# Kernel optimization log

Hardware: AMD Instinct MI355X
Metric: run time of the kernel (lower is better)

The kernel has to match this reference:

```python
import jax, jax.numpy as jnp
import numpy as np

H = 1024          # hidden_size
NH = 16           # num_attention_heads
HD = H // NH      # head_size
EPS = 1e-5


def setup_inputs() -> dict:
    key = jax.random.key(0)
    ks = jax.random.split(key, 5)
    # xavier_uniform bound for Linear(in, out): sqrt(6/(in+out))
    b_qkv = float(np.sqrt(6.0 / (H + 3 * H)))
    b_out = float(np.sqrt(6.0 / (H + H)))
    return {
        "hidden_states": jax.random.normal(ks[0], (2, 2048, H), dtype=jnp.float32),
        "ln_gamma": jnp.ones((H,), jnp.float32),
        "ln_beta": jnp.zeros((H,), jnp.float32),
        "W_qkv": jax.random.uniform(ks[1], (3 * H, H), jnp.float32, -b_qkv, b_qkv),
        "b_qkv": jnp.zeros((3 * H,), jnp.float32),
        "W_out": jax.random.uniform(ks[2], (H, H), jnp.float32, -b_out, b_out),
        "b_out": jnp.zeros((H,), jnp.float32),
    }


def _attn_block(x, ln_gamma, ln_beta, W_qkv, b_qkv, W_out, b_out):
    B, S, _ = x.shape
    # Pre-LN
    mu = jnp.mean(x, axis=-1, keepdims=True)
    var = jnp.mean(jnp.square(x - mu), axis=-1, keepdims=True)
    xn = (x - mu) / jnp.sqrt(var + EPS) * ln_gamma + ln_beta
    # fused QKV projection: [B,S,3H]
    qkv = jnp.einsum("bsh,oh->bso", xn, W_qkv) + b_qkv
    qkv = qkv.reshape(B, S, 3, NH, HD).transpose(2, 0, 3, 1, 4)  # [3,B,NH,S,HD]
    q, k, v = qkv[0], qkv[1], qkv[2]
    scores = jnp.einsum("bhqd,bhkd->bhqk", q, k) / jnp.sqrt(jnp.asarray(HD, x.dtype))
    probs = jax.nn.softmax(scores, axis=-1)
    ctx = jnp.einsum("bhqk,bhkd->bhqd", probs, v)
    ctx = ctx.transpose(0, 2, 1, 3).reshape(B, S, H)
    out = jnp.einsum("bsh,oh->bso", ctx, W_out) + b_out  # dropout: eval mode = identity
    return x + out


def reference(hidden_states, ln_gamma, ln_beta, W_qkv, b_qkv, W_out, b_out):
    return _attn_block(hidden_states, ln_gamma, ln_beta, W_qkv, b_qkv, W_out, b_out)
```

## Files before the change

### kernel.cpp

```cpp
#include <hip/hip_runtime.h>
#include <stdint.h>

typedef unsigned short u16;
typedef __attribute__((ext_vector_type(8))) short bf16x8;
typedef __attribute__((ext_vector_type(4))) float f32x4;
typedef __attribute__((ext_vector_type(16))) float f32x16;
typedef __attribute__((ext_vector_type(4))) unsigned int u32x4;
typedef __attribute__((ext_vector_type(2))) unsigned int u32x2;
typedef __attribute__((ext_vector_type(4))) unsigned short u16x4;

#define QSCALE 0.18033688011112042f

typedef __attribute__((address_space(1))) const void gvoid;
typedef __attribute__((address_space(3))) void svoid;

__device__ __forceinline__ void cp16(const u16* g, u16* l) {
    __builtin_amdgcn_global_load_lds((gvoid*)g, (svoid*)l, 16, 0, 0);
}

__device__ __forceinline__ u16 f2bf(float f) {
    uint32_t u = __float_as_uint(f);
    u += 0x7fff + ((u >> 16) & 1);
    return (u16)(u >> 16);
}

__device__ __forceinline__ uint32_t pack_bf2(float lo, float hi) {
    uint32_t a = __float_as_uint(lo) + 0x8000u;
    uint32_t b = __float_as_uint(hi) + 0x8000u;
    return __builtin_amdgcn_perm(b, a, 0x07060302);
}

__device__ __forceinline__ f32x16 zero16() {
    f32x16 v;
    #pragma unroll
    for (int i = 0; i < 16; i++) v[i] = 0.f;
    return v;
}

__global__ __launch_bounds__(256) void k_pre(const float* __restrict__ X,
                                             const float* __restrict__ gam,
                                             const float* __restrict__ bet,
                                             u16* __restrict__ XN,
                                             const float* __restrict__ Wqkv, u16* __restrict__ Wq,
                                             const float* __restrict__ Wout, u16* __restrict__ Wo) {
    __shared__ float red[8];
    const int bid = blockIdx.x;
    if (bid < 4096) {
        int t = bid;
        const float4* xp = (const float4*)(X + (size_t)t * 1024);
        float4 x = xp[threadIdx.x];
        float s  = x.x + x.y + x.z + x.w;
        float s2 = x.x*x.x + x.y*x.y + x.z*x.z + x.w*x.w;
        #pragma unroll
        for (int off = 1; off < 64; off <<= 1) {
            s  += __shfl_xor(s,  off, 64);
            s2 += __shfl_xor(s2, off, 64);
        }
        int lane = threadIdx.x & 63, w = threadIdx.x >> 6;
        if (lane == 0) { red[w] = s; red[w + 4] = s2; }
        __syncthreads();
        s  = red[0] + red[1] + red[2] + red[3];
        s2 = red[4] + red[5] + red[6] + red[7];
        float mu  = s * (1.0f / 1024.0f);
        float var = s2 * (1.0f / 1024.0f) - mu * mu;
        float rin = rsqrtf(var + 1e-5f);
        float4 g = ((const float4*)gam)[threadIdx.x];
        float4 b = ((const float4*)bet)[threadIdx.x];
        u16x4 o;
        o.x = f2bf((x.x - mu) * rin * g.x + b.x);
        o.y = f2bf((x.y - mu) * rin * g.y + b.y);
        o.z = f2bf((x.z - mu) * rin * g.z + b.z);
        o.w = f2bf((x.w - mu) * rin * g.w + b.w);
        *(u16x4*)(XN + (size_t)t * 1024 + threadIdx.x * 4) = o;
    } else {
        int i = (bid - 4096) * 256 + threadIdx.x;
        const float* src; u16* dst;
        if (i < 786432) { src = Wqkv; dst = Wq; }
        else            { i -= 786432; src = Wout; dst = Wo; }
        float4 v = ((const float4*)src)[i];
        u16x4 o;
        o.x = f2bf(v.x); o.y = f2bf(v.y); o.z = f2bf(v.z); o.w = f2bf(v.w);
        ((u16x4*)dst)[i] = o;
    }
}

__device__ __forceinline__ void gemm_bt_tile(const u16* __restrict__ A, const u16* __restrict__ Bm,
                                             int m0, int n0, u16* As, u16* Bs, f32x4 acc[4][4]) {
    const int tid = threadIdx.x;
    const int lane = tid & 63;
    const int wv = tid >> 6;
    const int qi = lane & 15, g = lane >> 4, swz = qi & 7;
    const int wr = (wv >> 1) * 64, wc = (wv & 1) * 64;
    #pragma unroll
    for (int mi = 0; mi < 4; mi++)
        #pragma unroll
        for (int ni = 0; ni < 4; ni++) acc[mi][ni] = (f32x4){0.f, 0.f, 0.f, 0.f};

    const int row_in = tid >> 3;
    const int cs = (tid & 7) ^ (row_in & 7);
    for (int k0 = 0; k0 < 1024; k0 += 64) {
        __syncthreads();
        #pragma unroll
        for (int i = 0; i < 4; i++) {
            int row = i * 32 + row_in;
            cp16(A  + (size_t)(m0 + row) * 1024 + k0 + cs * 8, As + (i * 256 + wv * 64) * 8);
            cp16(Bm + (size_t)(n0 + row) * 1024 + k0 + cs * 8, Bs + (i * 256 + wv * 64) * 8);
        }
        __syncthreads();
        #pragma unroll
        for (int ks = 0; ks < 2; ks++) {
            bf16x8 af[4], bf[4];
            #pragma unroll
            for (int mi = 0; mi < 4; mi++)
                af[mi] = *(const bf16x8*)(As + (wr + mi * 16 + qi) * 64 + ((ks * 4 + g) ^ swz) * 8);
            #pragma unroll
            for (int ni = 0; ni < 4; ni++)
                bf[ni] = *(const bf16x8*)(Bs + (wc + ni * 16 + qi) * 64 + ((ks * 4 + g) ^ swz) * 8);
            #pragma unroll
            for (int mi = 0; mi < 4; mi++)
                #pragma unroll
                for (int ni = 0; ni < 4; ni++)
                    acc[mi][ni] = __builtin_amdgcn_mfma_f32_16x16x32_bf16(af[mi], bf[ni], acc[mi][ni], 0, 0, 0);
        }
    }
}


#define CFENCE asm volatile("" ::: "memory")
#define BARX() do { CFENCE; __builtin_amdgcn_s_barrier(); CFENCE; } while (0)
#define LGKM0() asm volatile("s_waitcnt lgkmcnt(0)" ::: "memory")

__global__ __launch_bounds__(512, 2) void k_qkv(const u16* __restrict__ XN, const u16* __restrict__ Wq,
                                                const float* __restrict__ bqkv,
                                                u16* __restrict__ Q, u16* __restrict__ K,
                                                u16* __restrict__ Vt) {
    __shared__ __align__(16) u16 SMEM[65536];
    const int tid = threadIdx.x;
    const int lane = tid & 63, w = tid >> 6;
    const int qi = lane & 15, g = lane >> 4, swz = qi & 7;
    const int wr = (w >> 2) * 128, wc = (w & 3) * 64;

    const int id = blockIdx.x;
    const int sw = (id & 7) * 24 + (id >> 3);
    const int n0 = (sw % 12) * 256;
    const int m0 = (sw / 12) * 256;

    const int laneRow = lane >> 3, laneCg = lane & 7;
    const int cs = laneCg ^ laneRow;
    const int aw = (w & 3) * 8 + (w >> 2) * 128;
    const u16* gA = XN + (size_t)(m0 + aw + laneRow) * 1024 + cs * 8;
    const u16* gB = Wq + (size_t)(n0 + w * 8 + laneRow) * 1024 + cs * 8;

#define SM_A(s) (SMEM + (s) * 32768)
#define SM_B(s) (SMEM + (s) * 32768 + 16384)
#define STAGE_A(tau, q, s) cp16(gA + (size_t)(q) * 32 * 1024 + (tau) * 64, SM_A(s) + ((q) * 32 + aw) * 64)
#define STAGE_B(tau, part, s)                                                                       \
    do { cp16(gB + (size_t)(part) * 128 * 1024 + (tau) * 64, SM_B(s) + ((part) * 128 + w * 8) * 64); \
         cp16(gB + (size_t)((part) * 128 + 64) * 1024 + (tau) * 64,                                  \
              SM_B(s) + ((part) * 128 + 64 + w * 8) * 64); } while (0)

    f32x4 acc[8][4];
    #pragma unroll
    for (int mi = 0; mi < 8; mi++)
        #pragma unroll
        for (int ni = 0; ni < 4; ni++) acc[mi][ni] = (f32x4){0.f, 0.f, 0.f, 0.f};
    bf16x8 bf[4][2];

    STAGE_B(0, 0, 0); STAGE_B(0, 1, 0);
    STAGE_A(0, 0, 0); STAGE_A(0, 1, 0); STAGE_A(0, 2, 0); STAGE_A(0, 3, 0);
    STAGE_B(1, 0, 1); STAGE_B(1, 1, 1);
    STAGE_A(1, 0, 1); STAGE_A(1, 1, 1);
    asm volatile("s_waitcnt vmcnt(6)" ::: "memory");
    BARX();

#define PHASE_A(q)                                                                                   \
    bf16x8 af[2][2];                                                                                 \
    _Pragma("unroll") for (int m2 = 0; m2 < 2; m2++)                                                 \
    _Pragma("unroll") for (int ks = 0; ks < 2; ks++)                                                 \
        af[m2][ks] = *(const bf16x8*)(as_ + (wr + ((q) * 2 + m2) * 16 + qi) * 64 + (((ks * 4 + g) ^ swz)) * 8);

#define DO_MFMA(q)                                                                                   \
    __builtin_amdgcn_s_setprio(1);                                                                   \
    _Pragma("unroll") for (int m2 = 0; m2 < 2; m2++)                                                 \
    _Pragma("unroll") for (int ni = 0; ni < 4; ni++) {                                               \
        acc[(q) * 2 + m2][ni] = __builtin_amdgcn_mfma_f32_16x16x32_bf16(af[m2][0], bf[ni][0], acc[(q) * 2 + m2][ni], 0, 0, 0); \
        acc[(q) * 2 + m2][ni] = __builtin_amdgcn_mfma_f32_16x16x32_bf16(af[m2][1], bf[ni][1], acc[(q) * 2 + m2][ni], 0, 0, 0); \
    }                                                                                                \
    __builtin_amdgcn_s_setprio(0);

    for (int t = 0; t < 16; t++) {
        const int s = t & 1;
        const u16* as_ = SM_A(s);
        const u16* bs_ = SM_B(s);
        {
            PHASE_A(0)
            #pragma unroll
            for (int ni = 0; ni < 4; ni++)
                #pragma unroll
                for (int ks = 0; ks < 2; ks++)
                    bf[ni][ks] = *(const bf16x8*)(bs_ + (wc + ni * 16 + qi) * 64 + ((ks * 4 + g) ^ swz) * 8);
            if (t < 15) { STAGE_A(t + 1, 2, s ^ 1); STAGE_A(t + 1, 3, s ^ 1); }
            BARX(); LGKM0();
            DO_MFMA(0)
            BARX();
        }
        {
            PHASE_A(1)
            if (t < 14) STAGE_B(t + 2, 0, s);
            BARX(); LGKM0();
            DO_MFMA(1)
            BARX();
        }
        {
            PHASE_A(2)
            if (t < 14) STAGE_B(t + 2, 1, s);
            BARX(); LGKM0();
            DO_MFMA(2)
            BARX();
        }
        {
            PHASE_A(3)
            if (t < 14) { STAGE_A(t + 2, 0, s); STAGE_A(t + 2, 1, s); }
            BARX(); LGKM0();
            DO_MFMA(3)
            if (t < 14) { asm volatile("s_waitcnt vmcnt(6)" ::: "memory"); }
            else        { asm volatile("s_waitcnt vmcnt(0)" ::: "memory"); }
            BARX();
        }
    }

    if (n0 < 2048) {
        const int which = n0 >> 10;
        u16* base = which ? K : Q;
        const float scale = which ? 1.0f : QSCALE;
        #pragma unroll
        for (int mi = 0; mi < 8; mi++)
            #pragma unroll
            for (int ni = 0; ni < 4; ni++)
                #pragma unroll
                for (int i = 0; i < 4; i++) {
                    int m = m0 + wr + mi * 16 + (g * 4 + i);
                    int n = n0 + wc + ni * 16 + qi;
                    float v = (acc[mi][ni][i] + bqkv[n]) * scale;
                    int b = m >> 11, ss = m & 2047;
                    int hh = (n >> 6) & 15, d = n & 63;
                    base[((size_t)(b * 16 + hh) * 2048 + ss) * 64 + d] = f2bf(v);
                }
    } else {
        u16* Tw = SMEM + w * 4352;
        const int head = (n0 + wc - 2048) >> 6;
        const int b = m0 >> 11;
        #pragma unroll
        for (int h = 0; h < 2; h++) {
            #pragma unroll
            for (int mi2 = 0; mi2 < 4; mi2++)
                #pragma unroll
                for (int ni = 0; ni < 4; ni++) {
                    int mi = h * 4 + mi2;
                    int n = n0 + wc + ni * 16 + qi;
                    float bq = bqkv[n];
                    u16x4 pk;
                    pk.x = f2bf(acc[mi][ni][0] + bq);
                    pk.y = f2bf(acc[mi][ni][1] + bq);
                    pk.z = f2bf(acc[mi][ni][2] + bq);
                    pk.w = f2bf(acc[mi][ni][3] + bq);
                    *(u16x4*)(Tw + (ni * 16 + qi) * 68 + mi2 * 16 + g * 4) = pk;
                }
            int s0 = (m0 + wr + h * 64) & 2047;
            u16* vrow = Vt + (size_t)(b * 16 + head) * 64 * 2048 + s0 + qi * 4;
            #pragma unroll
            for (int dd = 0; dd < 16; dd++) {
                int d = dd * 4 + g;
                u16x4 val = *(const u16x4*)(Tw + d * 68 + qi * 4);
                *(u16x4*)(vrow + (size_t)d * 2048) = val;
            }
        }
    }
#undef SM_A
#undef SM_B
#undef STAGE_A
#undef STAGE_B
#undef PHASE_A
#undef DO_MFMA
}

__global__ __launch_bounds__(256) void k_attn(const u16* __restrict__ Q, const u16* __restrict__ K,
                                              const u16* __restrict__ Vt, u16* __restrict__ CTX) {
    __shared__ __align__(16) u16 Ks[2][64 * 64];
    __shared__ __align__(16) u16 Vs[2][64 * 64];
    const int id = blockIdx.x;
    const int bh = (id & 7) * 4 + ((id >> 3) & 3);
    const int q0 = (id >> 5) * 128;
    const int lane = threadIdx.x & 63, w = threadIdx.x >> 6;
    const int l = lane & 31, h = lane >> 5;
    const u16* Qp = Q  + (size_t)bh * (2048 * 64);
    const u16* Kp = K  + (size_t)bh * (2048 * 64);
    const u16* Vp = Vt + (size_t)bh * (64 * 2048);

    const int r0 = w * 8 + (lane >> 3);
    const int cs = (lane & 7) ^ (r0 & 7);
    const u16* kgp = Kp + (size_t)r0 * 64 + cs * 8;
    const u16* vgp = Vp + (size_t)r0 * 2048 + cs * 8;

    bf16x8 bq[4];
    {
        const u16* qb = Qp + (size_t)(q0 + w * 32 + l) * 64 + h * 8;
        #pragma unroll
        for (int dk = 0; dk < 4; dk++) bq[dk] = *(const bf16x8*)(qb + dk * 16);
    }
    float lsA = 0.f, lsB = 0.f;
    f32x16 od0 = zero16(), od1 = zero16();

    cp16(kgp,              Ks[0] + w * 512);
    cp16(kgp + 32 * 64,    Ks[0] + w * 512 + 2048);
    cp16(vgp,              Vs[0] + w * 512);
    cp16(vgp + 32 * 2048,  Vs[0] + w * 512 + 2048);

    for (int t = 0; t < 32; ++t) {
        __syncthreads();
        if (t < 31) {
            const int nb = (t + 1) & 1;
            cp16(kgp + 4096,             Ks[nb] + w * 512);
            cp16(kgp + 4096 + 32 * 64,   Ks[nb] + w * 512 + 2048);
            cp16(vgp + 64,               Vs[nb] + w * 512);
            cp16(vgp + 64 + 32 * 2048,   Vs[nb] + w * 512 + 2048);
        }
        kgp += 4096; vgp += 64;
        const u16* ksp = Ks[t & 1];
        const u16* vsp = Vs[t & 1];

        f32x16 sv0 = zero16(), sv1 = zero16();
        __builtin_amdgcn_s_setprio(1);
        #pragma unroll
        for (int dk = 0; dk < 4; dk++) {
            bf16x8 ak0 = *(const bf16x8*)(ksp + (l) * 64      + ((2 * dk + h) ^ (l & 7)) * 8);
            bf16x8 ak1 = *(const bf16x8*)(ksp + (32 + l) * 64 + ((2 * dk + h) ^ (l & 7)) * 8);
            sv0 = __builtin_amdgcn_mfma_f32_32x32x16_bf16(ak0, bq[dk], sv0, 0, 0, 0);
            sv1 = __builtin_amdgcn_mfma_f32_32x32x16_bf16(ak1, bq[dk], sv1, 0, 0, 0);
        }
        __builtin_amdgcn_s_setprio(0);

        uint32_t y[2][2][4];
#define SM_PACK(SV, KG, LS)                                                   \
        _Pragma("unroll")                                                     \
        for (int s = 0; s < 4; s++)                                           \
            _Pragma("unroll")                                                 \
            for (int p = 0; p < 2; p++) {                                     \
                float e0 = __builtin_amdgcn_exp2f(SV[4 * s + 2 * p]);         \
                float e1 = __builtin_amdgcn_exp2f(SV[4 * s + 2 * p + 1]);     \
                LS += e0 + e1;                                                \
                y[KG][p][s] = pack_bf2(e0, e1);                               \
            }
        SM_PACK(sv0, 0, lsA)
        SM_PACK(sv1, 1, lsB)
#undef SM_PACK

        #pragma unroll
        for (int m = 0; m < 4; m++) {
            const int kg = m >> 1, mt = m & 1;
            u32x2 r0s = __builtin_amdgcn_permlane32_swap(y[kg][0][2 * mt], y[kg][0][2 * mt + 1], false, false);
            u32x2 r1s = __builtin_amdgcn_permlane32_swap(y[kg][1][2 * mt], y[kg][1][2 * mt + 1], false, false);
            u32x4 bw = {r0s.x, r1s.x, r0s.y, r1s.y};
            bf16x8 bp = *(const bf16x8*)&bw;
            bf16x8 av0 = *(const bf16x8*)(vsp + (l) * 64      + ((2 * m + h) ^ (l & 7)) * 8);
            bf16x8 av1 = *(const bf16x8*)(vsp + (32 + l) * 64 + ((2 * m + h) ^ (l & 7)) * 8);
            __builtin_amdgcn_s_setprio(1);
            od0 = __builtin_amdgcn_mfma_f32_32x32x16_bf16(av0, bp, od0, 0, 0, 0);
            od1 = __builtin_amdgcn_mfma_f32_32x32x16_bf16(av1, bp, od1, 0, 0, 0);
            __builtin_amdgcn_s_setprio(0);
        }
    }

    float lsum = lsA + lsB;
    lsum += __shfl_xor(lsum, 32, 64);
    float inv = 1.0f / lsum;
    const int b = bh >> 4, hh = bh & 15;
    size_t m = (size_t)b * 2048 + q0 + w * 32 + l;
    u16* cp = CTX + m * 1024 + hh * 64;
    #pragma unroll
    for (int s = 0; s < 4; s++) {
        u16x4 o;
        o.x = f2bf(od0[4 * s + 0] * inv); o.y = f2bf(od0[4 * s + 1] * inv);
        o.z = f2bf(od0[4 * s + 2] * inv); o.w = f2bf(od0[4 * s + 3] * inv);
        *(u16x4*)(cp + 8 * s + 4 * h) = o;
        o.x = f2bf(od1[4 * s + 0] * inv); o.y = f2bf(od1[4 * s + 1] * inv);
        o.z = f2bf(od1[4 * s + 2] * inv); o.w = f2bf(od1[4 * s + 3] * inv);
        *(u16x4*)(cp + 32 + 8 * s + 4 * h) = o;
    }
}

__global__ __launch_bounds__(256) void k_out(const u16* __restrict__ CTX, const u16* __restrict__ Wo,
                                             const float* __restrict__ bout, const float* __restrict__ X,
                                             float* __restrict__ OUT) {
    __shared__ __align__(16) u16 As[128 * 64], Bs[128 * 64];
    f32x4 acc[4][4];
    const int m0 = blockIdx.y * 128, n0 = blockIdx.x * 128;
    gemm_bt_tile(CTX, Wo, m0, n0, As, Bs, acc);
    const int lane = threadIdx.x & 63, wid = threadIdx.x >> 6;
    const int wr = (wid >> 1) * 64, wc = (wid & 1) * 64;
    #pragma unroll
    for (int mi = 0; mi < 4; mi++)
        #pragma unroll
        for (int ni = 0; ni < 4; ni++)
            #pragma unroll
            for (int i = 0; i < 4; i++) {
                size_t m = m0 + wr + mi * 16 + ((lane >> 4) * 4 + i);
                int n = n0 + wc + ni * 16 + (lane & 15);
                OUT[m * 1024 + n] = acc[mi][ni][i] + bout[n] + X[m * 1024 + n];
            }
}

extern "C" void kernel_launch(void* const* d_in, const int* in_sizes, int n_in,
                              void* d_out, int out_size, void* d_ws, size_t ws_size,
                              hipStream_t stream) {
    const float* X    = (const float*)d_in[0];
    const float* gam  = (const float*)d_in[1];
    const float* bet  = (const float*)d_in[2];
    const float* Wqkv = (const float*)d_in[3];
    const float* bqkv = (const float*)d_in[4];
    const float* Wout = (const float*)d_in[5];
    const float* bout = (const float*)d_in[6];
    float* OUT = (float*)d_out;

    u16* XN  = (u16*)d_ws;
    u16* Q   = XN  + (size_t)4 * 1024 * 1024;
    u16* K   = Q   + (size_t)4 * 1024 * 1024;
    u16* Vt  = K   + (size_t)4 * 1024 * 1024;
    u16* CTX = Vt  + (size_t)4 * 1024 * 1024;
    u16* Wq  = CTX + (size_t)4 * 1024 * 1024;
    u16* Wo  = Wq  + (size_t)3 * 1024 * 1024;

    k_pre<<<8192, 256, 0, stream>>>(X, gam, bet, XN, Wqkv, Wq, Wout, Wo);
    k_qkv<<<192, 512, 0, stream>>>(XN, Wq, bqkv, Q, K, Vt);
    k_attn<<<512, 256, 0, stream>>>(Q, K, Vt, CTX);
    k_out<<<dim3(8, 32), 256, 0, stream>>>(CTX, Wo, bout, X, OUT);
}
```

Before: 194.6 us.

## Split attention key tile across wave pairs and double the grid

Each attention block now handles 64 queries instead of 128. The two waves sharing a 32-query group each process half of every 64-key tile. Their partial outputs and row sums are reduced through shared memory at the end, and the grid is doubled to 1024 blocks with a launch bound of 4 blocks per SIMD. This raises parallelism and occupancy on the 256-CU part, but each block now reloads the full K/V stream for only half as many queries, which doubles global K/V traffic and adds a reduction step.

```diff
diff --git a/kernel.cpp b/kernel.cpp
--- a/kernel.cpp
+++ b/kernel.cpp
@@ -284,15 +284,16 @@
 #undef DO_MFMA
 }
 
-__global__ __launch_bounds__(256) void k_attn(const u16* __restrict__ Q, const u16* __restrict__ K,
-                                              const u16* __restrict__ Vt, u16* __restrict__ CTX) {
+__global__ __launch_bounds__(256, 4) void k_attn(const u16* __restrict__ Q, const u16* __restrict__ K,
+                                                 const u16* __restrict__ Vt, u16* __restrict__ CTX) {
     __shared__ __align__(16) u16 Ks[2][64 * 64];
     __shared__ __align__(16) u16 Vs[2][64 * 64];
     const int id = blockIdx.x;
     const int bh = (id & 7) * 4 + ((id >> 3) & 3);
-    const int q0 = (id >> 5) * 128;
+    const int q0 = (id >> 5) * 64;
     const int lane = threadIdx.x & 63, w = threadIdx.x >> 6;
     const int l = lane & 31, h = lane >> 5;
+    const int qg = w >> 1, kh = w & 1;
     const u16* Qp = Q  + (size_t)bh * (2048 * 64);
     const u16* Kp = K  + (size_t)bh * (2048 * 64);
     const u16* Vp = Vt + (size_t)bh * (64 * 2048);
@@ -304,11 +305,11 @@
 
     bf16x8 bq[4];
     {
-        const u16* qb = Qp + (size_t)(q0 + w * 32 + l) * 64 + h * 8;
+        const u16* qb = Qp + (size_t)(q0 + qg * 32 + l) * 64 + h * 8;
         #pragma unroll
         for (int dk = 0; dk < 4; dk++) bq[dk] = *(const bf16x8*)(qb + dk * 16);
     }
-    float lsA = 0.f, lsB = 0.f;
+    float ls = 0.f;
     f32x16 od0 = zero16(), od1 = zero16();
 
     cp16(kgp,              Ks[0] + w * 512);
@@ -329,41 +330,34 @@
         const u16* ksp = Ks[t & 1];
         const u16* vsp = Vs[t & 1];
 
-        f32x16 sv0 = zero16(), sv1 = zero16();
+        f32x16 sv = zero16();
         __builtin_amdgcn_s_setprio(1);
         #pragma unroll
         for (int dk = 0; dk < 4; dk++) {
-            bf16x8 ak0 = *(const bf16x8*)(ksp + (l) * 64      + ((2 * dk + h) ^ (l & 7)) * 8);
-            bf16x8 ak1 = *(const bf16x8*)(ksp + (32 + l) * 64 + ((2 * dk + h) ^ (l & 7)) * 8);
-            sv0 = __builtin_amdgcn_mfma_f32_32x32x16_bf16(ak0, bq[dk], sv0, 0, 0, 0);
-            sv1 = __builtin_amdgcn_mfma_f32_32x32x16_bf16(ak1, bq[dk], sv1, 0, 0, 0);
+            bf16x8 ak = *(const bf16x8*)(ksp + (kh * 32 + l) * 64 + ((2 * dk + h) ^ (l & 7)) * 8);
+            sv = __builtin_amdgcn_mfma_f32_32x32x16_bf16(ak, bq[dk], sv, 0, 0, 0);
         }
         __builtin_amdgcn_s_setprio(0);
 
-        uint32_t y[2][2][4];
-#define SM_PACK(SV, KG, LS)                                                   \
-        _Pragma("unroll")                                                     \
-        for (int s = 0; s < 4; s++)                                           \
-            _Pragma("unroll")                                                 \
-            for (int p = 0; p < 2; p++) {                                     \
-                float e0 = __builtin_amdgcn_exp2f(SV[4 * s + 2 * p]);         \
-                float e1 = __builtin_amdgcn_exp2f(SV[4 * s + 2 * p + 1]);     \
-                LS += e0 + e1;                                                \
-                y[KG][p][s] = pack_bf2(e0, e1);                               \
+        uint32_t y[2][4];
+        #pragma unroll
+        for (int s = 0; s < 4; s++)
+            #pragma unroll
+            for (int p = 0; p < 2; p++) {
+                float e0 = __builtin_amdgcn_exp2f(sv[4 * s + 2 * p]);
+                float e1 = __builtin_amdgcn_exp2f(sv[4 * s + 2 * p + 1]);
+                ls += e0 + e1;
+                y[p][s] = pack_bf2(e0, e1);
             }
-        SM_PACK(sv0, 0, lsA)
-        SM_PACK(sv1, 1, lsB)
-#undef SM_PACK
-
-        #pragma unroll
-        for (int m = 0; m < 4; m++) {
-            const int kg = m >> 1, mt = m & 1;
-            u32x2 r0s = __builtin_amdgcn_permlane32_swap(y[kg][0][2 * mt], y[kg][0][2 * mt + 1], false, false);
-            u32x2 r1s = __builtin_amdgcn_permlane32_swap(y[kg][1][2 * mt], y[kg][1][2 * mt + 1], false, false);
+
+        #pragma unroll
+        for (int mt = 0; mt < 2; mt++) {
+            u32x2 r0s = __builtin_amdgcn_permlane32_swap(y[0][2 * mt], y[0][2 * mt + 1], false, false);
+            u32x2 r1s = __builtin_amdgcn_permlane32_swap(y[1][2 * mt], y[1][2 * mt + 1], false, false);
             u32x4 bw = {r0s.x, r1s.x, r0s.y, r1s.y};
             bf16x8 bp = *(const bf16x8*)&bw;
-            bf16x8 av0 = *(const bf16x8*)(vsp + (l) * 64      + ((2 * m + h) ^ (l & 7)) * 8);
-            bf16x8 av1 = *(const bf16x8*)(vsp + (32 + l) * 64 + ((2 * m + h) ^ (l & 7)) * 8);
+            bf16x8 av0 = *(const bf16x8*)(vsp + (l) * 64      + ((kh * 4 + 2 * mt + h) ^ (l & 7)) * 8);
+            bf16x8 av1 = *(const bf16x8*)(vsp + (32 + l) * 64 + ((kh * 4 + 2 * mt + h) ^ (l & 7)) * 8);
             __builtin_amdgcn_s_setprio(1);
             od0 = __builtin_amdgcn_mfma_f32_32x32x16_bf16(av0, bp, od0, 0, 0, 0);
             od1 = __builtin_amdgcn_mfma_f32_32x32x16_bf16(av1, bp, od1, 0, 0, 0);
@@ -371,21 +365,43 @@
         }
     }
 
-    float lsum = lsA + lsB;
-    lsum += __shfl_xor(lsum, 32, 64);
-    float inv = 1.0f / lsum;
-    const int b = bh >> 4, hh = bh & 15;
-    size_t m = (size_t)b * 2048 + q0 + w * 32 + l;
-    u16* cp = CTX + m * 1024 + hh * 64;
-    #pragma unroll
-    for (int s = 0; s < 4; s++) {
-        u16x4 o;
-        o.x = f2bf(od0[4 * s + 0] * inv); o.y = f2bf(od0[4 * s + 1] * inv);
-        o.z = f2bf(od0[4 * s + 2] * inv); o.w = f2bf(od0[4 * s + 3] * inv);
-        *(u16x4*)(cp + 8 * s + 4 * h) = o;
-        o.x = f2bf(od1[4 * s + 0] * inv); o.y = f2bf(od1[4 * s + 1] * inv);
-        o.z = f2bf(od1[4 * s + 2] * inv); o.w = f2bf(od1[4 * s + 3] * inv);
-        *(u16x4*)(cp + 32 + 8 * s + 4 * h) = o;
+    __syncthreads();
+    float* cb  = (float*)&Ks[0][0];
+    float* lsb = (float*)&Vs[0][0];
+    if (kh == 1) {
+        #pragma unroll
+        for (int c = 0; c < 8; c++) {
+            f32x4 v;
+            if (c < 4) { v.x = od0[4*c+0]; v.y = od0[4*c+1]; v.z = od0[4*c+2]; v.w = od0[4*c+3]; }
+            else       { v.x = od1[4*(c-4)+0]; v.y = od1[4*(c-4)+1]; v.z = od1[4*(c-4)+2]; v.w = od1[4*(c-4)+3]; }
+            *(f32x4*)(cb + qg * 2048 + lane * 32 + (c ^ (lane & 7)) * 4) = v;
+        }
+        lsb[qg * 64 + lane] = ls;
+    }
+    __syncthreads();
+    if (kh == 0) {
+        #pragma unroll
+        for (int c = 0; c < 8; c++) {
+            f32x4 v = *(const f32x4*)(cb + qg * 2048 + lane * 32 + (c ^ (lane & 7)) * 4);
+            if (c < 4) { od0[4*c+0] += v.x; od0[4*c+1] += v.y; od0[4*c+2] += v.z; od0[4*c+3] += v.w; }
+            else       { od1[4*(c-4)+0] += v.x; od1[4*(c-4)+1] += v.y; od1[4*(c-4)+2] += v.z; od1[4*(c-4)+3] += v.w; }
+        }
+        ls += lsb[qg * 64 + lane];
+        float lsum = ls + __shfl_xor(ls, 32, 64);
+        float inv = 1.0f / lsum;
+        const int b = bh >> 4, hh = bh & 15;
+        size_t m = (size_t)b * 2048 + q0 + qg * 32 + l;
+        u16* cp = CTX + m * 1024 + hh * 64;
+        #pragma unroll
+        for (int s = 0; s < 4; s++) {
+            u16x4 o;
+            o.x = f2bf(od0[4 * s + 0] * inv); o.y = f2bf(od0[4 * s + 1] * inv);
+            o.z = f2bf(od0[4 * s + 2] * inv); o.w = f2bf(od0[4 * s + 3] * inv);
+            *(u16x4*)(cp + 8 * s + 4 * h) = o;
+            o.x = f2bf(od1[4 * s + 0] * inv); o.y = f2bf(od1[4 * s + 1] * inv);
+            o.z = f2bf(od1[4 * s + 2] * inv); o.w = f2bf(od1[4 * s + 3] * inv);
+            *(u16x4*)(cp + 32 + 8 * s + 4 * h) = o;
+        }
     }
 }
 
@@ -432,6 +448,6 @@
 
     k_pre<<<8192, 256, 0, stream>>>(X, gam, bet, XN, Wqkv, Wq, Wout, Wo);
     k_qkv<<<192, 512, 0, stream>>>(XN, Wq, bqkv, Q, K, Vt);
-    k_attn<<<512, 256, 0, stream>>>(Q, K, Vt, CTX);
+    k_attn<<<1024, 256, 0, stream>>>(Q, K, Vt, CTX);
     k_out<<<dim3(8, 32), 256, 0, stream>>>(CTX, Wo, bout, X, OUT);
 }
```

Result: no change. 193.9 us (-0.4%).
